# Kernel tuning notes

Hardware: AMD Instinct MI355X
Metric: run time of the kernel (lower is better)

Reference implementation:

```python
import jax, jax.numpy as jnp
import numpy as np

B, S, E, H = 8, 2048, 1024, 4
D = E // H  # per-head attention embed_dim (torch MHA with num_heads=1)


def setup_inputs() -> dict:
    key = jax.random.key(0)
    ks = jax.random.split(key, 7)
    scale = 0.02
    return {
        "x": jax.random.normal(ks[0], (B, S, E), dtype=jnp.float32),
        # outer linear: torch Linear(E, E) -> y = x @ W.T + b
        "W_lin": jax.random.normal(ks[1], (E, E), dtype=jnp.float32) * scale,
        "b_lin": jnp.zeros((E,), dtype=jnp.float32),
        # per-head MultiheadAttention params, stacked over H heads
        # in_proj: [3D, D] weight, [3D] bias per head (q,k,v stacked)
        "W_in": jax.random.normal(ks[2], (H, 3 * D, D), dtype=jnp.float32) * scale,
        "b_in": jnp.zeros((H, 3 * D), dtype=jnp.float32),
        # out_proj: [D, D] weight, [D] bias per head
        "W_out": jax.random.normal(ks[3], (H, D, D), dtype=jnp.float32) * scale,
        "b_out": jnp.zeros((H, D), dtype=jnp.float32),
    }


def _forward(x, W_lin, b_lin, W_in, b_in, W_out, b_out):
    # outer projection
    x_proj = jnp.einsum("bse,fe->bsf", x, W_lin) + b_lin          # [B,S,E]
    # torch.chunk(dim=-1) into H contiguous slices of width D == reshape
    xs = x_proj.reshape(B, S, H, D)                                 # [B,S,H,D]
    # per-head in_proj (q,k,v share input; weights stacked as [3D, D])
    qkv = jnp.einsum("bshd,hed->bshe", xs, W_in) + b_in             # [B,S,H,3D]
    q, k, v = jnp.split(qkv, 3, axis=-1)                            # each [B,S,H,D]
    # scaled dot-product attention per head (inner num_heads=1 -> head dim D)
    scores = jnp.einsum("bshd,bthd->bhst", q, k) / jnp.sqrt(jnp.float32(D))
    attn = jax.nn.softmax(scores, axis=-1)                          # [B,H,S,S]
    out = jnp.einsum("bhst,bthd->bshd", attn, v)                    # [B,S,H,D]
    # per-head out_proj
    out = jnp.einsum("bshd,hed->bshe", out, W_out) + b_out          # [B,S,H,D]
    # concat heads back along feature dim
    return out.reshape(B, S, E)


def reference(x, W_lin, b_lin, W_in, b_in, W_out, b_out):
    return _forward(x, W_lin, b_lin, W_in, b_in, W_out, b_out)
```

## Files before the change

### kernel.cpp

```cpp
#include <hip/hip_runtime.h>


typedef unsigned short u16;
typedef short s8v __attribute__((ext_vector_type(8)));
typedef float f4v __attribute__((ext_vector_type(4)));
typedef unsigned short us8v __attribute__((ext_vector_type(8)));

typedef const __attribute__((address_space(1))) void* gas_t;
typedef __attribute__((address_space(3))) void* las_t;

__device__ __forceinline__ u16 f2bf(float f) {
  unsigned u = __builtin_bit_cast(unsigned, f);
  unsigned r = u + 0x7FFFu + ((u >> 16) & 1u);
  return (u16)(r >> 16);
}

__device__ __forceinline__ void gload16(const void* g, void* l) {
  __builtin_amdgcn_global_load_lds((gas_t)g, (las_t)l, 16, 0, 0);
}

__global__ void cast_kernel(const float* __restrict__ in, u16* __restrict__ out, int n4) {
  int i = blockIdx.x * blockDim.x + threadIdx.x;
  const int stride = gridDim.x * blockDim.x;
  for (; i < n4; i += stride) {
    const float4 v = reinterpret_cast<const float4*>(in)[i];
    ushort4 o;
    o.x = f2bf(v.x); o.y = f2bf(v.y); o.z = f2bf(v.z); o.w = f2bf(v.w);
    reinterpret_cast<ushort4*>(out)[i] = o;
  }
}

template <int MODE>
__global__ void __launch_bounds__(256, 2) gemm128(
    const u16* __restrict__ A, const u16* __restrict__ Bw,
    const float* __restrict__ bias,
    u16* __restrict__ outB, float* __restrict__ outF,
    u16* __restrict__ Qo, u16* __restrict__ Ko, u16* __restrict__ Vo)
{
  constexpr int K    = (MODE == 0) ? 1024 : 256;
  constexpr int LDA  = 1024;
  constexpr int LDB  = (MODE == 0) ? 1024 : 256;
  constexpr int SMEM = (MODE == 1) ? 35072 : 32768;

  const int bx = blockIdx.x, ny = blockIdx.y, h = blockIdx.z;
  const int tid = threadIdx.x;
  const int wid = tid >> 6, l = tid & 63;
  const int l15 = l & 15, lg = l >> 4;
  const int wr = wid >> 1, wc = wid & 1;

  __shared__ __align__(16) char smem[SMEM];
  char* Al = smem;
  char* Bl = smem + 16384;

  const u16* Abase = A + (size_t)bx * 128 * LDA + ((MODE == 0) ? 0 : h * 256);
  const size_t bwoff = (MODE == 0) ? 0
                      : ((MODE == 1) ? (size_t)h * 768 * 256 : (size_t)h * 256 * 256);
  const u16* Bbase = Bw + bwoff + (size_t)ny * 128 * LDB;

  f4v acc[4][4];
#pragma unroll
  for (int i = 0; i < 4; ++i)
#pragma unroll
    for (int j = 0; j < 4; ++j) acc[i][j] = f4v{0.f, 0.f, 0.f, 0.f};

  for (int k0 = 0; k0 < K; k0 += 64) {
    __syncthreads();
#pragma unroll
    for (int ii = 0; ii < 4; ++ii) {
      const int i = wid * 4 + ii;
      const int row = i * 8 + (l >> 3);
      const int c = l & 7;
      gload16(Abase + (size_t)row * LDA + k0 + ((c ^ (row & 7)) << 3), Al + i * 1024);
    }
#pragma unroll
    for (int ii = 0; ii < 4; ++ii) {
      const int i = wid * 4 + ii;
      const int row = i * 8 + (l >> 3);
      const int c = l & 7;
      gload16(Bbase + (size_t)row * LDB + k0 + ((c ^ (row & 7)) << 3), Bl + i * 1024);
    }
    __syncthreads();
#pragma unroll
    for (int kf = 0; kf < 2; ++kf) {
      s8v a[4];
#pragma unroll
      for (int mf = 0; mf < 4; ++mf) {
        const int row = wr * 64 + mf * 16 + l15;
        a[mf] = *reinterpret_cast<const s8v*>(
            Al + row * 128 + (((kf * 32 + lg * 8) << 1) ^ ((row & 7) << 4)));
      }
#pragma unroll
      for (int nf = 0; nf < 4; ++nf) {
        const int n = wc * 64 + nf * 16 + l15;
        const s8v b = *reinterpret_cast<const s8v*>(
            Bl + n * 128 + (((kf * 32 + lg * 8) << 1) ^ ((n & 7) << 4)));
#pragma unroll
        for (int mf = 0; mf < 4; ++mf)
          acc[mf][nf] = __builtin_amdgcn_mfma_f32_16x16x32_bf16(a[mf], b, acc[mf][nf], 0, 0, 0);
      }
    }
  }

  const int mbase = bx * 128 + wr * 64;
  const int nbase = ny * 128 + wc * 64;

  if constexpr (MODE == 0) {
#pragma unroll
    for (int nf = 0; nf < 4; ++nf) {
      const int colg = nbase + nf * 16 + l15;
      const float bv = bias[colg];
#pragma unroll
      for (int mf = 0; mf < 4; ++mf)
#pragma unroll
        for (int r = 0; r < 4; ++r) {
          const int mr = mbase + mf * 16 + lg * 4 + r;
          outB[(size_t)mr * 1024 + colg] = f2bf(acc[mf][nf][r] + bv);
        }
    }
  } else if constexpr (MODE == 2) {
#pragma unroll
    for (int nf = 0; nf < 4; ++nf) {
      const int colg = nbase + nf * 16 + l15;
      const float bv = bias[h * 256 + colg];
#pragma unroll
      for (int mf = 0; mf < 4; ++mf)
#pragma unroll
        for (int r = 0; r < 4; ++r) {
          const int mr = mbase + mf * 16 + lg * 4 + r;
          outF[(size_t)mr * 1024 + h * 256 + colg] = acc[mf][nf][r] + bv;
        }
    }
  } else {
    if (ny < 4) {
      u16* dst = (ny < 2) ? Qo : Ko;
      const int cb = (ny < 2) ? 0 : 256;
#pragma unroll
      for (int nf = 0; nf < 4; ++nf) {
        const int colg = nbase + nf * 16 + l15;
        const float bv = bias[h * 768 + colg];
        const int d = colg - cb;
#pragma unroll
        for (int mf = 0; mf < 4; ++mf)
#pragma unroll
          for (int r = 0; r < 4; ++r) {
            const int mr = mbase + mf * 16 + lg * 4 + r;
            const int b = mr >> 11, s = mr & 2047;
            dst[((size_t)(b * 4 + h) * 2048 + s) * 256 + d] = f2bf(acc[mf][nf][r] + bv);
          }
      }
    } else {
      __syncthreads();
      short* tr = reinterpret_cast<short*>(smem);
#pragma unroll
      for (int nf = 0; nf < 4; ++nf) {
        const int colg = nbase + nf * 16 + l15;
        const float bv = bias[h * 768 + colg];
        const int cl = wc * 64 + nf * 16 + l15;
#pragma unroll
        for (int mf = 0; mf < 4; ++mf)
#pragma unroll
          for (int r = 0; r < 4; ++r) {
            const int rl = wr * 64 + mf * 16 + lg * 4 + r;
            tr[rl * 137 + cl] = (short)f2bf(acc[mf][nf][r] + bv);
          }
      }
      __syncthreads();
      const int b = bx >> 4;
      const int sbase = (bx & 15) * 128;
#pragma unroll
      for (int rep = 0; rep < 8; ++rep) {
        const int u = rep * 256 + tid;
        const int d = u >> 4, sb = u & 15;
        us8v v;
#pragma unroll
        for (int j = 0; j < 8; ++j) v[j] = (u16)tr[(sb * 8 + j) * 137 + d];
        *reinterpret_cast<us8v*>(
            Vo + ((size_t)(b * 4 + h) * 256 + (ny - 4) * 128 + d) * 2048 + sbase + sb * 8) = v;
      }
    }
  }
}

__global__ void __launch_bounds__(256, 2) attn_fwd(
    const u16* __restrict__ Q, const u16* __restrict__ Kk,
    const u16* __restrict__ Vt, u16* __restrict__ AO)
{
  const int bh = blockIdx.y;
  const int qt = blockIdx.x;
  const int tid = threadIdx.x;
  const int wid = tid >> 6, l = tid & 63;
  const int l15 = l & 15, lg = l >> 4;

  __shared__ __align__(16) char smem[32768 + 32768 + 9216];
  char* Kl = smem;
  char* Vl = smem + 32768;
  short* Pl = reinterpret_cast<short*>(smem + 65536) + wid * 1152;

  s8v qa[8];
  {
    const u16* qrow = Q + ((size_t)bh * 2048 + qt * 64 + wid * 16 + l15) * 256;
#pragma unroll
    for (int kf = 0; kf < 8; ++kf)
      qa[kf] = *reinterpret_cast<const s8v*>(qrow + kf * 32 + lg * 8);
  }

  f4v O[16];
#pragma unroll
  for (int i = 0; i < 16; ++i) O[i] = f4v{0.f, 0.f, 0.f, 0.f};
  float m_run[4] = {-3e38f, -3e38f, -3e38f, -3e38f};
  float l_run[4] = {0.f, 0.f, 0.f, 0.f};

  const size_t kbase = (size_t)bh * 2048 * 256;
  const size_t vbase = (size_t)bh * 256 * 2048;

  for (int t0 = 0; t0 < 2048; t0 += 64) {
    __syncthreads();
#pragma unroll
    for (int ii = 0; ii < 8; ++ii) {
      const int i = wid * 8 + ii;
      const int row = i * 2 + (l >> 5);
      const int c = l & 31;
      gload16(Kk + kbase + (size_t)(t0 + row) * 256 + ((c ^ (row & 7)) << 3), Kl + i * 1024);
    }
#pragma unroll
    for (int ii = 0; ii < 8; ++ii) {
      const int i = wid * 8 + ii;
      const int d = i * 8 + (l >> 3);
      const int c = l & 7;
      gload16(Vt + vbase + (size_t)d * 2048 + t0 + ((c ^ (d & 7)) << 3), Vl + i * 1024);
    }
    __syncthreads();

    f4v S[4];
#pragma unroll
    for (int i = 0; i < 4; ++i) S[i] = f4v{0.f, 0.f, 0.f, 0.f};
#pragma unroll
    for (int kf = 0; kf < 8; ++kf) {
#pragma unroll
      for (int nf = 0; nf < 4; ++nf) {
        const int tl = nf * 16 + l15;
        const s8v kb = *reinterpret_cast<const s8v*>(
            Kl + tl * 512 + (((kf * 32 + lg * 8) << 1) ^ ((tl & 7) << 4)));
        S[nf] = __builtin_amdgcn_mfma_f32_16x16x32_bf16(qa[kf], kb, S[nf], 0, 0, 0);
      }
    }

    float fac[4];
#pragma unroll
    for (int r = 0; r < 4; ++r) {
      const float s0 = S[0][r] * 0.0625f;
      const float s1 = S[1][r] * 0.0625f;
      const float s2 = S[2][r] * 0.0625f;
      const float s3 = S[3][r] * 0.0625f;
      float mx = fmaxf(fmaxf(s0, s1), fmaxf(s2, s3));
      mx = fmaxf(mx, __shfl_xor(mx, 1));
      mx = fmaxf(mx, __shfl_xor(mx, 2));
      mx = fmaxf(mx, __shfl_xor(mx, 4));
      mx = fmaxf(mx, __shfl_xor(mx, 8));
      const float m_new = fmaxf(m_run[r], mx);
      fac[r] = __expf(m_run[r] - m_new);
      m_run[r] = m_new;
      const float p0 = __expf(s0 - m_new);
      const float p1 = __expf(s1 - m_new);
      const float p2 = __expf(s2 - m_new);
      const float p3 = __expf(s3 - m_new);
      float rs = p0 + p1 + p2 + p3;
      rs += __shfl_xor(rs, 1);
      rs += __shfl_xor(rs, 2);
      rs += __shfl_xor(rs, 4);
      rs += __shfl_xor(rs, 8);
      l_run[r] = l_run[r] * fac[r] + rs;
      short* pr = Pl + (lg * 4 + r) * 72;
      pr[l15]      = (short)f2bf(p0);
      pr[16 + l15] = (short)f2bf(p1);
      pr[32 + l15] = (short)f2bf(p2);
      pr[48 + l15] = (short)f2bf(p3);
    }

#pragma unroll
    for (int df = 0; df < 16; ++df) {
      O[df][0] *= fac[0]; O[df][1] *= fac[1];
      O[df][2] *= fac[2]; O[df][3] *= fac[3];
    }

    __syncthreads();

    s8v pa[2];
#pragma unroll
    for (int kf2 = 0; kf2 < 2; ++kf2)
      pa[kf2] = *reinterpret_cast<const s8v*>(Pl + l15 * 72 + kf2 * 32 + lg * 8);

#pragma unroll
    for (int kf2 = 0; kf2 < 2; ++kf2) {
#pragma unroll
      for (int df = 0; df < 16; ++df) {
        const int dl = df * 16 + l15;
        const s8v vb = *reinterpret_cast<const s8v*>(
            Vl + dl * 128 + (((kf2 * 32 + lg * 8) << 1) ^ ((dl & 7) << 4)));
        O[df] = __builtin_amdgcn_mfma_f32_16x16x32_bf16(pa[kf2], vb, O[df], 0, 0, 0);
      }
    }
  }

  float inv[4];
#pragma unroll
  for (int r = 0; r < 4; ++r) inv[r] = 1.0f / l_run[r];
  const int b = bh >> 2, h = bh & 3;
#pragma unroll
  for (int df = 0; df < 16; ++df)
#pragma unroll
    for (int r = 0; r < 4; ++r) {
      const int srow = qt * 64 + wid * 16 + lg * 4 + r;
      AO[(size_t)(b * 2048 + srow) * 1024 + h * 256 + df * 16 + l15] = f2bf(O[df][r] * inv[r]);
    }
}

extern "C" void kernel_launch(void* const* d_in, const int* in_sizes, int n_in,
                              void* d_out, int out_size, void* d_ws, size_t ws_size,
                              hipStream_t stream) {
  (void)in_sizes; (void)n_in; (void)out_size; (void)ws_size;
  const float* x     = (const float*)d_in[0];
  const float* W_lin = (const float*)d_in[1];
  const float* b_lin = (const float*)d_in[2];
  const float* W_in  = (const float*)d_in[3];
  const float* b_in  = (const float*)d_in[4];
  const float* W_out = (const float*)d_in[5];
  const float* b_out = (const float*)d_in[6];

  char* ws = (char*)d_ws;
  u16* Qb  = (u16*)(ws);
  u16* Vtb = (u16*)(ws + (32ull << 20));
  u16* AOb = (u16*)(ws + (64ull << 20));
  u16* WLb = (u16*)(ws + (96ull << 20));
  u16* WIb = (u16*)(ws + (98ull << 20));
  u16* WOb = (u16*)(ws + (98ull << 20) + 1572864ull);

  char* doc  = (char*)d_out;
  u16* xb    = (u16*)doc;
  u16* xproj = (u16*)(doc + (32ull << 20));
  u16* Kb    = (u16*)doc;
  float* outF = (float*)d_out;

  cast_kernel<<<2048, 256, 0, stream>>>(x, xb, 4194304);
  cast_kernel<<<1024, 256, 0, stream>>>(W_lin, WLb, 262144);
  cast_kernel<<<768, 256, 0, stream>>>(W_in, WIb, 196608);
  cast_kernel<<<256, 256, 0, stream>>>(W_out, WOb, 65536);

  gemm128<0><<<dim3(128, 8, 1), 256, 0, stream>>>(xb, WLb, b_lin, xproj, nullptr,
                                                  nullptr, nullptr, nullptr);
  gemm128<1><<<dim3(128, 6, 4), 256, 0, stream>>>(xproj, WIb, b_in, nullptr, nullptr,
                                                  Qb, Kb, Vtb);
  attn_fwd<<<dim3(32, 32, 1), 256, 0, stream>>>(Qb, Kb, Vtb, AOb);
  gemm128<2><<<dim3(128, 2, 4), 256, 0, stream>>>(AOb, WOb, b_out, nullptr, outF,
                                                  nullptr, nullptr, nullptr);
}
```

Baseline: 398.4 us.

## Double-buffer attention K/V tiles, widen Q tile, lazy rescale, fold scale into weights

The attention kernel now handles 128 query rows per block (two 16-row fragments per wave) over 32-key tiles. K/V tiles are double-buffered so the next tile's global-to-LDS load overlaps the current tile's compute, which leaves one barrier per iteration. The softmax skips rescaling O unless some row's max grows by more than 8, and the 1/sqrt(D) scale is folded into the Q slice of W_in and its bias during casting. This cuts K/V reloads and per-tile exp/multiply work, at the cost of more registers per wave and fewer blocks in the grid.

Result: slower. 544.8 us (+36.7%).

```diff
diff --git a/kernel.cpp b/kernel.cpp
--- a/kernel.cpp
+++ b/kernel.cpp
@@ -28,6 +28,16 @@
     o.x = f2bf(v.x); o.y = f2bf(v.y); o.z = f2bf(v.z); o.w = f2bf(v.w);
     reinterpret_cast<ushort4*>(out)[i] = o;
   }
+}
+
+__global__ void cast_win(const float* __restrict__ in, u16* __restrict__ out, int n4) {
+  const int i = blockIdx.x * blockDim.x + threadIdx.x;
+  if (i >= n4) return;
+  const float4 v = reinterpret_cast<const float4*>(in)[i];
+  const float sc = (((i >> 6) % 768) < 256) ? 0.0625f : 1.0f;
+  ushort4 o;
+  o.x = f2bf(v.x * sc); o.y = f2bf(v.y * sc); o.z = f2bf(v.z * sc); o.w = f2bf(v.w * sc);
+  reinterpret_cast<ushort4*>(out)[i] = o;
 }
 
 template <int MODE>
@@ -134,10 +144,11 @@
     if (ny < 4) {
       u16* dst = (ny < 2) ? Qo : Ko;
       const int cb = (ny < 2) ? 0 : 256;
+      const float bscale = (ny < 2) ? 0.0625f : 1.0f;
 #pragma unroll
       for (int nf = 0; nf < 4; ++nf) {
         const int colg = nbase + nf * 16 + l15;
-        const float bv = bias[h * 768 + colg];
+        const float bv = bias[h * 768 + colg] * bscale;
         const int d = colg - cb;
 #pragma unroll
         for (int mf = 0; mf < 4; ++mf)
@@ -191,128 +202,163 @@
   const int wid = tid >> 6, l = tid & 63;
   const int l15 = l & 15, lg = l >> 4;
 
-  __shared__ __align__(16) char smem[32768 + 32768 + 9216];
-  char* Kl = smem;
-  char* Vl = smem + 32768;
-  short* Pl = reinterpret_cast<short*>(smem + 65536) + wid * 1152;
-
-  s8v qa[8];
-  {
-    const u16* qrow = Q + ((size_t)bh * 2048 + qt * 64 + wid * 16 + l15) * 256;
-#pragma unroll
-    for (int kf = 0; kf < 8; ++kf)
-      qa[kf] = *reinterpret_cast<const s8v*>(qrow + kf * 32 + lg * 8);
-  }
-
-  f4v O[16];
-#pragma unroll
-  for (int i = 0; i < 16; ++i) O[i] = f4v{0.f, 0.f, 0.f, 0.f};
-  float m_run[4] = {-3e38f, -3e38f, -3e38f, -3e38f};
-  float l_run[4] = {0.f, 0.f, 0.f, 0.f};
+  __shared__ __align__(16) char smem[75776];
+  short* Pl = reinterpret_cast<short*>(smem + 65536 + wid * 2560);
 
   const size_t kbase = (size_t)bh * 2048 * 256;
   const size_t vbase = (size_t)bh * 256 * 2048;
 
-  for (int t0 = 0; t0 < 2048; t0 += 64) {
-    __syncthreads();
-#pragma unroll
-    for (int ii = 0; ii < 8; ++ii) {
-      const int i = wid * 8 + ii;
+  s8v qa[2][8];
+#pragma unroll
+  for (int mf = 0; mf < 2; ++mf) {
+    const u16* qrow = Q + ((size_t)bh * 2048 + qt * 128 + wid * 32 + mf * 16 + l15) * 256;
+#pragma unroll
+    for (int kf = 0; kf < 8; ++kf)
+      qa[mf][kf] = *reinterpret_cast<const s8v*>(qrow + kf * 32 + lg * 8);
+  }
+
+  f4v O[2][16];
+#pragma unroll
+  for (int mf = 0; mf < 2; ++mf)
+#pragma unroll
+    for (int df = 0; df < 16; ++df) O[mf][df] = f4v{0.f, 0.f, 0.f, 0.f};
+  float m_run[2][4], l_run[2][4];
+#pragma unroll
+  for (int mf = 0; mf < 2; ++mf)
+#pragma unroll
+    for (int r = 0; r < 4; ++r) { m_run[mf][r] = -1e30f; l_run[mf][r] = 0.f; }
+
+  auto stage = [&](int t0, int cur) {
+#pragma unroll
+    for (int ii = 0; ii < 4; ++ii) {
+      const int i = wid * 4 + ii;
       const int row = i * 2 + (l >> 5);
       const int c = l & 31;
-      gload16(Kk + kbase + (size_t)(t0 + row) * 256 + ((c ^ (row & 7)) << 3), Kl + i * 1024);
-    }
-#pragma unroll
-    for (int ii = 0; ii < 8; ++ii) {
-      const int i = wid * 8 + ii;
-      const int d = i * 8 + (l >> 3);
-      const int c = l & 7;
-      gload16(Vt + vbase + (size_t)d * 2048 + t0 + ((c ^ (d & 7)) << 3), Vl + i * 1024);
-    }
+      gload16(Kk + kbase + (size_t)(t0 + row) * 256 + ((c ^ (row & 7)) << 3),
+              smem + cur * 16384 + i * 1024);
+    }
+#pragma unroll
+    for (int ii = 0; ii < 4; ++ii) {
+      const int i = wid * 4 + ii;
+      const int d = i * 16 + (l >> 2);
+      const int c = l & 3;
+      gload16(Vt + vbase + (size_t)d * 2048 + t0 + ((c ^ ((d >> 1) & 3)) << 3),
+              smem + 32768 + cur * 16384 + i * 1024);
+    }
+  };
+
+  stage(0, 0);
+  __syncthreads();
+
+  for (int t = 0; t < 64; ++t) {
+    const int cur = t & 1;
+    if (t < 63) stage((t + 1) * 32, cur ^ 1);
+
+    const char* Kl = smem + cur * 16384;
+    const char* Vl = smem + 32768 + cur * 16384;
+
+    f4v S[2][2];
+#pragma unroll
+    for (int mf = 0; mf < 2; ++mf)
+#pragma unroll
+      for (int nf = 0; nf < 2; ++nf) S[mf][nf] = f4v{0.f, 0.f, 0.f, 0.f};
+
+#pragma unroll
+    for (int kf = 0; kf < 8; ++kf) {
+      const int ch = kf * 4 + lg;
+      const int t0l = l15, t1l = 16 + l15;
+      const s8v kb0 = *reinterpret_cast<const s8v*>(Kl + t0l * 512 + ((ch ^ (t0l & 7)) << 4));
+      const s8v kb1 = *reinterpret_cast<const s8v*>(Kl + t1l * 512 + ((ch ^ (t1l & 7)) << 4));
+      S[0][0] = __builtin_amdgcn_mfma_f32_16x16x32_bf16(qa[0][kf], kb0, S[0][0], 0, 0, 0);
+      S[1][0] = __builtin_amdgcn_mfma_f32_16x16x32_bf16(qa[1][kf], kb0, S[1][0], 0, 0, 0);
+      S[0][1] = __builtin_amdgcn_mfma_f32_16x16x32_bf16(qa[0][kf], kb1, S[0][1], 0, 0, 0);
+      S[1][1] = __builtin_amdgcn_mfma_f32_16x16x32_bf16(qa[1][kf], kb1, S[1][1], 0, 0, 0);
+    }
+
+    float mxv[2][4];
+#pragma unroll
+    for (int mf = 0; mf < 2; ++mf)
+#pragma unroll
+      for (int r = 0; r < 4; ++r) {
+        float mx = fmaxf(S[mf][0][r], S[mf][1][r]);
+        mx = fmaxf(mx, __shfl_xor(mx, 1));
+        mx = fmaxf(mx, __shfl_xor(mx, 2));
+        mx = fmaxf(mx, __shfl_xor(mx, 4));
+        mx = fmaxf(mx, __shfl_xor(mx, 8));
+        mxv[mf][r] = mx;
+      }
+    bool need = false;
+#pragma unroll
+    for (int mf = 0; mf < 2; ++mf)
+#pragma unroll
+      for (int r = 0; r < 4; ++r)
+        need = need || (mxv[mf][r] > m_run[mf][r] + 8.f);
+    if (__any(need)) {
+#pragma unroll
+      for (int mf = 0; mf < 2; ++mf)
+#pragma unroll
+        for (int r = 0; r < 4; ++r) {
+          const float mn = fmaxf(m_run[mf][r], mxv[mf][r]);
+          const float fac = __expf(m_run[mf][r] - mn);
+          m_run[mf][r] = mn;
+          l_run[mf][r] *= fac;
+#pragma unroll
+          for (int df = 0; df < 16; ++df) O[mf][df][r] *= fac;
+        }
+    }
+
+#pragma unroll
+    for (int mf = 0; mf < 2; ++mf)
+#pragma unroll
+      for (int r = 0; r < 4; ++r) {
+        const float p0 = __expf(S[mf][0][r] - m_run[mf][r]);
+        const float p1 = __expf(S[mf][1][r] - m_run[mf][r]);
+        float rs = p0 + p1;
+        rs += __shfl_xor(rs, 1);
+        rs += __shfl_xor(rs, 2);
+        rs += __shfl_xor(rs, 4);
+        rs += __shfl_xor(rs, 8);
+        l_run[mf][r] += rs;
+        short* pr = Pl + (mf * 16 + lg * 4 + r) * 40;
+        pr[l15]      = (short)f2bf(p0);
+        pr[16 + l15] = (short)f2bf(p1);
+      }
+
+    asm volatile("s_waitcnt lgkmcnt(0)" ::: "memory");
+    __builtin_amdgcn_sched_barrier(0);
+
+    s8v pa[2];
+#pragma unroll
+    for (int mf = 0; mf < 2; ++mf)
+      pa[mf] = *reinterpret_cast<const s8v*>(Pl + (mf * 16 + l15) * 40 + lg * 8);
+
+#pragma unroll
+    for (int df = 0; df < 16; ++df) {
+      const int dl = df * 16 + l15;
+      const s8v vb = *reinterpret_cast<const s8v*>(
+          Vl + dl * 64 + ((lg ^ ((dl >> 1) & 3)) << 4));
+      O[0][df] = __builtin_amdgcn_mfma_f32_16x16x32_bf16(pa[0], vb, O[0][df], 0, 0, 0);
+      O[1][df] = __builtin_amdgcn_mfma_f32_16x16x32_bf16(pa[1], vb, O[1][df], 0, 0, 0);
+    }
+
     __syncthreads();
-
-    f4v S[4];
-#pragma unroll
-    for (int i = 0; i < 4; ++i) S[i] = f4v{0.f, 0.f, 0.f, 0.f};
-#pragma unroll
-    for (int kf = 0; kf < 8; ++kf) {
-#pragma unroll
-      for (int nf = 0; nf < 4; ++nf) {
-        const int tl = nf * 16 + l15;
-        const s8v kb = *reinterpret_cast<const s8v*>(
-            Kl + tl * 512 + (((kf * 32 + lg * 8) << 1) ^ ((tl & 7) << 4)));
-        S[nf] = __builtin_amdgcn_mfma_f32_16x16x32_bf16(qa[kf], kb, S[nf], 0, 0, 0);
-      }
-    }
-
-    float fac[4];
-#pragma unroll
-    for (int r = 0; r < 4; ++r) {
-      const float s0 = S[0][r] * 0.0625f;
-      const float s1 = S[1][r] * 0.0625f;
-      const float s2 = S[2][r] * 0.0625f;
-      const float s3 = S[3][r] * 0.0625f;
-      float mx = fmaxf(fmaxf(s0, s1), fmaxf(s2, s3));
-      mx = fmaxf(mx, __shfl_xor(mx, 1));
-      mx = fmaxf(mx, __shfl_xor(mx, 2));
-      mx = fmaxf(mx, __shfl_xor(mx, 4));
-      mx = fmaxf(mx, __shfl_xor(mx, 8));
-      const float m_new = fmaxf(m_run[r], mx);
-      fac[r] = __expf(m_run[r] - m_new);
-      m_run[r] = m_new;
-      const float p0 = __expf(s0 - m_new);
-      const float p1 = __expf(s1 - m_new);
-      const float p2 = __expf(s2 - m_new);
-      const float p3 = __expf(s3 - m_new);
-      float rs = p0 + p1 + p2 + p3;
-      rs += __shfl_xor(rs, 1);
-      rs += __shfl_xor(rs, 2);
-      rs += __shfl_xor(rs, 4);
-      rs += __shfl_xor(rs, 8);
-      l_run[r] = l_run[r] * fac[r] + rs;
-      short* pr = Pl + (lg * 4 + r) * 72;
-      pr[l15]      = (short)f2bf(p0);
-      pr[16 + l15] = (short)f2bf(p1);
-      pr[32 + l15] = (short)f2bf(p2);
-      pr[48 + l15] = (short)f2bf(p3);
-    }
-
-#pragma unroll
-    for (int df = 0; df < 16; ++df) {
-      O[df][0] *= fac[0]; O[df][1] *= fac[1];
-      O[df][2] *= fac[2]; O[df][3] *= fac[3];
-    }
-
-    __syncthreads();
-
-    s8v pa[2];
-#pragma unroll
-    for (int kf2 = 0; kf2 < 2; ++kf2)
-      pa[kf2] = *reinterpret_cast<const s8v*>(Pl + l15 * 72 + kf2 * 32 + lg * 8);
-
-#pragma unroll
-    for (int kf2 = 0; kf2 < 2; ++kf2) {
-#pragma unroll
-      for (int df = 0; df < 16; ++df) {
-        const int dl = df * 16 + l15;
-        const s8v vb = *reinterpret_cast<const s8v*>(
-            Vl + dl * 128 + (((kf2 * 32 + lg * 8) << 1) ^ ((dl & 7) << 4)));
-        O[df] = __builtin_amdgcn_mfma_f32_16x16x32_bf16(pa[kf2], vb, O[df], 0, 0, 0);
-      }
-    }
-  }
-
-  float inv[4];
-#pragma unroll
-  for (int r = 0; r < 4; ++r) inv[r] = 1.0f / l_run[r];
+  }
+
   const int b = bh >> 2, h = bh & 3;
 #pragma unroll
-  for (int df = 0; df < 16; ++df)
-#pragma unroll
-    for (int r = 0; r < 4; ++r) {
-      const int srow = qt * 64 + wid * 16 + lg * 4 + r;
-      AO[(size_t)(b * 2048 + srow) * 1024 + h * 256 + df * 16 + l15] = f2bf(O[df][r] * inv[r]);
-    }
+  for (int mf = 0; mf < 2; ++mf) {
+    float inv[4];
+#pragma unroll
+    for (int r = 0; r < 4; ++r) inv[r] = 1.0f / l_run[mf][r];
+#pragma unroll
+    for (int df = 0; df < 16; ++df)
+#pragma unroll
+      for (int r = 0; r < 4; ++r) {
+        const int srow = qt * 128 + wid * 32 + mf * 16 + lg * 4 + r;
+        AO[(size_t)(b * 2048 + srow) * 1024 + h * 256 + df * 16 + l15] =
+            f2bf(O[mf][df][r] * inv[r]);
+      }
+  }
 }
 
 extern "C" void kernel_launch(void* const* d_in, const int* in_sizes, int n_in,
@@ -343,14 +389,14 @@
 
   cast_kernel<<<2048, 256, 0, stream>>>(x, xb, 4194304);
   cast_kernel<<<1024, 256, 0, stream>>>(W_lin, WLb, 262144);
-  cast_kernel<<<768, 256, 0, stream>>>(W_in, WIb, 196608);
+  cast_win<<<768, 256, 0, stream>>>(W_in, WIb, 196608);
   cast_kernel<<<256, 256, 0, stream>>>(W_out, WOb, 65536);
 
   gemm128<0><<<dim3(128, 8, 1), 256, 0, stream>>>(xb, WLb, b_lin, xproj, nullptr,
                                                   nullptr, nullptr, nullptr);
   gemm128<1><<<dim3(128, 6, 4), 256, 0, stream>>>(xproj, WIb, b_in, nullptr, nullptr,
                                                   Qb, Kb, Vtb);
-  attn_fwd<<<dim3(32, 32, 1), 256, 0, stream>>>(Qb, Kb, Vtb, AOb);
+  attn_fwd<<<dim3(16, 32, 1), 256, 0, stream>>>(Qb, Kb, Vtb, AOb);
   gemm128<2><<<dim3(128, 2, 4), 256, 0, stream>>>(AOb, WOb, b_out, nullptr, outF,
                                                   nullptr, nullptr, nullptr);
 }
```

## Keep attention probabilities in registers via transposed S and lazy max rescaling

Applied to the files above, without the earlier changes.

Folds the softmax scale and log2(e) into the Q projection weights and bias so the attention kernel can use exp2 without a multiply. The score MFMA operands are swapped so each lane holds a full column of scores, which lets P be packed to bf16 in registers with v_cvt_pk_bf16_f32 and fed to the PV MFMA directly. This removes the LDS round-trip and one barrier per tile. Online-softmax rescaling of O is skipped unless the running max grows by more than a threshold, and V is stored in per-tile blocks with a permuted key order that matches the register P layout. The deferred rescaling lets unnormalized probabilities grow large, and the P layout depends on the exact MFMA register mapping.

Measured after the change: 330.3 us. 1.21x faster.

```diff
diff --git a/kernel.cpp b/kernel.cpp
--- a/kernel.cpp
+++ b/kernel.cpp
@@ -9,10 +9,18 @@
 typedef const __attribute__((address_space(1))) void* gas_t;
 typedef __attribute__((address_space(3))) void* las_t;
 
+#define QSCALE 0.09016844f
+
 __device__ __forceinline__ u16 f2bf(float f) {
   unsigned u = __builtin_bit_cast(unsigned, f);
   unsigned r = u + 0x7FFFu + ((u >> 16) & 1u);
   return (u16)(r >> 16);
+}
+
+__device__ __forceinline__ unsigned cvtpk(float a, float b) {
+  unsigned r;
+  asm("v_cvt_pk_bf16_f32 %0, %1, %2" : "=v"(r) : "v"(a), "v"(b));
+  return r;
 }
 
 __device__ __forceinline__ void gload16(const void* g, void* l) {
@@ -28,6 +36,16 @@
     o.x = f2bf(v.x); o.y = f2bf(v.y); o.z = f2bf(v.z); o.w = f2bf(v.w);
     reinterpret_cast<ushort4*>(out)[i] = o;
   }
+}
+
+__global__ void cast_win(const float* __restrict__ in, u16* __restrict__ out, int n4) {
+  const int i = blockIdx.x * blockDim.x + threadIdx.x;
+  if (i >= n4) return;
+  const float4 v = reinterpret_cast<const float4*>(in)[i];
+  const float sc = (((i >> 6) % 768) < 256) ? QSCALE : 1.0f;
+  ushort4 o;
+  o.x = f2bf(v.x * sc); o.y = f2bf(v.y * sc); o.z = f2bf(v.z * sc); o.w = f2bf(v.w * sc);
+  reinterpret_cast<ushort4*>(out)[i] = o;
 }
 
 template <int MODE>
@@ -134,10 +152,11 @@
     if (ny < 4) {
       u16* dst = (ny < 2) ? Qo : Ko;
       const int cb = (ny < 2) ? 0 : 256;
+      const float bscale = (ny < 2) ? QSCALE : 1.0f;
 #pragma unroll
       for (int nf = 0; nf < 4; ++nf) {
         const int colg = nbase + nf * 16 + l15;
-        const float bv = bias[h * 768 + colg];
+        const float bv = bias[h * 768 + colg] * bscale;
         const int d = colg - cb;
 #pragma unroll
         for (int mf = 0; mf < 4; ++mf)
@@ -166,16 +185,26 @@
       }
       __syncthreads();
       const int b = bx >> 4;
-      const int sbase = (bx & 15) * 128;
 #pragma unroll
       for (int rep = 0; rep < 8; ++rep) {
         const int u = rep * 256 + tid;
         const int d = u >> 4, sb = u & 15;
-        us8v v;
-#pragma unroll
-        for (int j = 0; j < 8; ++j) v[j] = (u16)tr[(sb * 8 + j) * 137 + d];
-        *reinterpret_cast<us8v*>(
-            Vo + ((size_t)(b * 4 + h) * 256 + (ny - 4) * 128 + d) * 2048 + sbase + sb * 8) = v;
+        const int dglob = (ny - 4) * 128 + d;
+        const int tile = (bx & 15) * 2 + (sb >> 3);
+        const int c = sb & 7;
+        const int kA = 32 * (c >> 2) + 8 * ((2 * c) & 3) + 4 * ((c >> 1) & 1);
+        u16* base = Vo + (((size_t)(b * 4 + h) * 32 + tile) * 256 + dglob) * 64;
+        ushort4 lo, hi;
+        lo.x = (u16)tr[(sb * 8 + 0) * 137 + d];
+        lo.y = (u16)tr[(sb * 8 + 1) * 137 + d];
+        lo.z = (u16)tr[(sb * 8 + 2) * 137 + d];
+        lo.w = (u16)tr[(sb * 8 + 3) * 137 + d];
+        hi.x = (u16)tr[(sb * 8 + 4) * 137 + d];
+        hi.y = (u16)tr[(sb * 8 + 5) * 137 + d];
+        hi.z = (u16)tr[(sb * 8 + 6) * 137 + d];
+        hi.w = (u16)tr[(sb * 8 + 7) * 137 + d];
+        *reinterpret_cast<ushort4*>(base + kA)     = lo;
+        *reinterpret_cast<ushort4*>(base + kA + 8) = hi;
       }
     }
   }
@@ -185,16 +214,17 @@
     const u16* __restrict__ Q, const u16* __restrict__ Kk,
     const u16* __restrict__ Vt, u16* __restrict__ AO)
 {
+  const int qt = blockIdx.x;
   const int bh = blockIdx.y;
-  const int qt = blockIdx.x;
   const int tid = threadIdx.x;
   const int wid = tid >> 6, l = tid & 63;
   const int l15 = l & 15, lg = l >> 4;
 
-  __shared__ __align__(16) char smem[32768 + 32768 + 9216];
+  __shared__ __align__(16) char smem[65536];
   char* Kl = smem;
   char* Vl = smem + 32768;
-  short* Pl = reinterpret_cast<short*>(smem + 65536) + wid * 1152;
+
+  const size_t kbase = (size_t)bh * 2048 * 256;
 
   s8v qa[8];
   {
@@ -206,12 +236,8 @@
 
   f4v O[16];
 #pragma unroll
-  for (int i = 0; i < 16; ++i) O[i] = f4v{0.f, 0.f, 0.f, 0.f};
-  float m_run[4] = {-3e38f, -3e38f, -3e38f, -3e38f};
-  float l_run[4] = {0.f, 0.f, 0.f, 0.f};
-
-  const size_t kbase = (size_t)bh * 2048 * 256;
-  const size_t vbase = (size_t)bh * 256 * 2048;
+  for (int df = 0; df < 16; ++df) O[df] = f4v{0.f, 0.f, 0.f, 0.f};
+  float m_run = -1e30f, l_run = 0.f;
 
   for (int t0 = 0; t0 < 2048; t0 += 64) {
     __syncthreads();
@@ -222,96 +248,105 @@
       const int c = l & 31;
       gload16(Kk + kbase + (size_t)(t0 + row) * 256 + ((c ^ (row & 7)) << 3), Kl + i * 1024);
     }
-#pragma unroll
-    for (int ii = 0; ii < 8; ++ii) {
-      const int i = wid * 8 + ii;
-      const int d = i * 8 + (l >> 3);
-      const int c = l & 7;
-      gload16(Vt + vbase + (size_t)d * 2048 + t0 + ((c ^ (d & 7)) << 3), Vl + i * 1024);
+    {
+      const u16* vtile = Vt + ((size_t)bh * 32 + (t0 >> 6)) * 16384;
+#pragma unroll
+      for (int ii = 0; ii < 8; ++ii) {
+        const int i = wid * 8 + ii;
+        const int d = i * 8 + (l >> 3);
+        const int c = l & 7;
+        gload16(vtile + (size_t)d * 64 + ((c ^ (d & 7)) << 3), Vl + i * 1024);
+      }
     }
     __syncthreads();
 
-    f4v S[4];
-#pragma unroll
-    for (int i = 0; i < 4; ++i) S[i] = f4v{0.f, 0.f, 0.f, 0.f};
+    f4v Sx[4];
+#pragma unroll
+    for (int nf = 0; nf < 4; ++nf) Sx[nf] = f4v{0.f, 0.f, 0.f, 0.f};
 #pragma unroll
     for (int kf = 0; kf < 8; ++kf) {
+      const int ch = kf * 4 + lg;
 #pragma unroll
       for (int nf = 0; nf < 4; ++nf) {
         const int tl = nf * 16 + l15;
         const s8v kb = *reinterpret_cast<const s8v*>(
-            Kl + tl * 512 + (((kf * 32 + lg * 8) << 1) ^ ((tl & 7) << 4)));
-        S[nf] = __builtin_amdgcn_mfma_f32_16x16x32_bf16(qa[kf], kb, S[nf], 0, 0, 0);
-      }
-    }
-
-    float fac[4];
-#pragma unroll
-    for (int r = 0; r < 4; ++r) {
-      const float s0 = S[0][r] * 0.0625f;
-      const float s1 = S[1][r] * 0.0625f;
-      const float s2 = S[2][r] * 0.0625f;
-      const float s3 = S[3][r] * 0.0625f;
-      float mx = fmaxf(fmaxf(s0, s1), fmaxf(s2, s3));
-      mx = fmaxf(mx, __shfl_xor(mx, 1));
-      mx = fmaxf(mx, __shfl_xor(mx, 2));
-      mx = fmaxf(mx, __shfl_xor(mx, 4));
-      mx = fmaxf(mx, __shfl_xor(mx, 8));
-      const float m_new = fmaxf(m_run[r], mx);
-      fac[r] = __expf(m_run[r] - m_new);
-      m_run[r] = m_new;
-      const float p0 = __expf(s0 - m_new);
-      const float p1 = __expf(s1 - m_new);
-      const float p2 = __expf(s2 - m_new);
-      const float p3 = __expf(s3 - m_new);
-      float rs = p0 + p1 + p2 + p3;
-      rs += __shfl_xor(rs, 1);
-      rs += __shfl_xor(rs, 2);
-      rs += __shfl_xor(rs, 4);
-      rs += __shfl_xor(rs, 8);
-      l_run[r] = l_run[r] * fac[r] + rs;
-      short* pr = Pl + (lg * 4 + r) * 72;
-      pr[l15]      = (short)f2bf(p0);
-      pr[16 + l15] = (short)f2bf(p1);
-      pr[32 + l15] = (short)f2bf(p2);
-      pr[48 + l15] = (short)f2bf(p3);
-    }
-
-#pragma unroll
-    for (int df = 0; df < 16; ++df) {
-      O[df][0] *= fac[0]; O[df][1] *= fac[1];
-      O[df][2] *= fac[2]; O[df][3] *= fac[3];
-    }
-
-    __syncthreads();
+            Kl + tl * 512 + ((ch ^ (tl & 7)) << 4));
+        Sx[nf] = __builtin_amdgcn_mfma_f32_16x16x32_bf16(kb, qa[kf], Sx[nf], 0, 0, 0);
+      }
+    }
+
+    float mloc = -1e30f;
+#pragma unroll
+    for (int nf = 0; nf < 4; ++nf)
+#pragma unroll
+      for (int r = 0; r < 4; ++r) mloc = fmaxf(mloc, Sx[nf][r]);
+    mloc = fmaxf(mloc, __shfl_xor(mloc, 16));
+    mloc = fmaxf(mloc, __shfl_xor(mloc, 32));
+
+    if (__any(mloc > m_run + 11.5f)) {
+      const float mn = fmaxf(m_run, mloc);
+      const float fac = __builtin_exp2f(m_run - mn);
+      m_run = mn;
+      l_run *= fac;
+      float facr[4];
+#pragma unroll
+      for (int r = 0; r < 4; ++r) facr[r] = __shfl(fac, lg * 4 + r);
+#pragma unroll
+      for (int df = 0; df < 16; ++df) {
+        O[df][0] *= facr[0]; O[df][1] *= facr[1];
+        O[df][2] *= facr[2]; O[df][3] *= facr[3];
+      }
+    }
+
+    float p[4][4];
+    float sum = 0.f;
+#pragma unroll
+    for (int nf = 0; nf < 4; ++nf)
+#pragma unroll
+      for (int r = 0; r < 4; ++r) {
+        p[nf][r] = __builtin_exp2f(Sx[nf][r] - m_run);
+        sum += p[nf][r];
+      }
+    sum += __shfl_xor(sum, 16);
+    sum += __shfl_xor(sum, 32);
+    l_run += sum;
 
     s8v pa[2];
 #pragma unroll
-    for (int kf2 = 0; kf2 < 2; ++kf2)
-      pa[kf2] = *reinterpret_cast<const s8v*>(Pl + l15 * 72 + kf2 * 32 + lg * 8);
-
-#pragma unroll
     for (int kf2 = 0; kf2 < 2; ++kf2) {
+      int4 w;
+      w.x = (int)cvtpk(p[2 * kf2][0],     p[2 * kf2][1]);
+      w.y = (int)cvtpk(p[2 * kf2][2],     p[2 * kf2][3]);
+      w.z = (int)cvtpk(p[2 * kf2 + 1][0], p[2 * kf2 + 1][1]);
+      w.w = (int)cvtpk(p[2 * kf2 + 1][2], p[2 * kf2 + 1][3]);
+      pa[kf2] = __builtin_bit_cast(s8v, w);
+    }
+
+#pragma unroll
+    for (int kf2 = 0; kf2 < 2; ++kf2) {
+      const int ch = kf2 * 4 + lg;
 #pragma unroll
       for (int df = 0; df < 16; ++df) {
         const int dl = df * 16 + l15;
         const s8v vb = *reinterpret_cast<const s8v*>(
-            Vl + dl * 128 + (((kf2 * 32 + lg * 8) << 1) ^ ((dl & 7) << 4)));
+            Vl + dl * 128 + ((ch ^ (dl & 7)) << 4));
         O[df] = __builtin_amdgcn_mfma_f32_16x16x32_bf16(pa[kf2], vb, O[df], 0, 0, 0);
       }
     }
   }
 
-  float inv[4];
-#pragma unroll
-  for (int r = 0; r < 4; ++r) inv[r] = 1.0f / l_run[r];
+  const float inv = 1.0f / l_run;
+  float invr[4];
+#pragma unroll
+  for (int r = 0; r < 4; ++r) invr[r] = __shfl(inv, lg * 4 + r);
   const int b = bh >> 2, h = bh & 3;
 #pragma unroll
   for (int df = 0; df < 16; ++df)
 #pragma unroll
     for (int r = 0; r < 4; ++r) {
       const int srow = qt * 64 + wid * 16 + lg * 4 + r;
-      AO[(size_t)(b * 2048 + srow) * 1024 + h * 256 + df * 16 + l15] = f2bf(O[df][r] * inv[r]);
+      AO[(size_t)(b * 2048 + srow) * 1024 + h * 256 + df * 16 + l15] =
+          f2bf(O[df][r] * invr[r]);
     }
 }
 
@@ -343,7 +378,7 @@
 
   cast_kernel<<<2048, 256, 0, stream>>>(x, xb, 4194304);
   cast_kernel<<<1024, 256, 0, stream>>>(W_lin, WLb, 262144);
-  cast_kernel<<<768, 256, 0, stream>>>(W_in, WIb, 196608);
+  cast_win<<<768, 256, 0, stream>>>(W_in, WIb, 196608);
   cast_kernel<<<256, 256, 0, stream>>>(W_out, WOb, 65536);
 
   gemm128<0><<<dim3(128, 8, 1), 256, 0, stream>>>(xb, WLb, b_lin, xproj, nullptr,
```
